# Performance work log

Hardware: AMD Instinct MI355X
Metric: run time of the kernel (lower is better)

## Reference

```python
import jax, jax.numpy as jnp
import numpy as np

N, E, F_IN, C, H, G = 50000, 800000, 128, 64, 4, 512

def _gat_layer(x, src, dst, W, a_src, a_dst, b):
    # x: [N, Fin]; W: [Fin, H*C]; a_src/a_dst: [H, C]; b: [C]
    n = x.shape[0]
    h = (x @ W).reshape(n, H, C)                      # [N,H,C]
    al_s = jnp.einsum('nhc,hc->nh', h, a_src)         # [N,H]
    al_d = jnp.einsum('nhc,hc->nh', h, a_dst)
    alpha = jax.nn.leaky_relu(al_s[src] + al_d[dst], 0.2)   # [Et,H]
    m = jax.ops.segment_max(alpha, dst, num_segments=n)      # segment softmax over dst
    e = jnp.exp(alpha - m[dst])
    s = jax.ops.segment_sum(e, dst, num_segments=n)
    coef = e / (s[dst] + 1e-16)                        # [Et,H]
    msg = h[src] * coef[:, :, None]                    # [Et,H,C]
    out = jax.ops.segment_sum(msg, dst, num_segments=n)
    return out.mean(axis=1) + b                        # concat=False: average heads

def setup_inputs():
    key = jax.random.key(0)
    ks = jax.random.split(key, 24)
    x = jax.random.normal(ks[0], (N, F_IN), jnp.float32)
    edge_index = jax.random.randint(ks[1], (2, E), 0, N, jnp.int64)
    edge_attr = jax.random.normal(ks[2], (E, 4), jnp.float32)
    batch_index = jnp.sort(jax.random.randint(ks[3], (N,), 0, G, jnp.int64))
    p = lambda k, shp: jax.random.normal(k, shp, jnp.float32) * 0.05
    inp = {
        'x': x, 'edge_index': edge_index, 'edge_attr': edge_attr, 'batch_index': batch_index,
        'W0': p(ks[4], (F_IN, H * C)), 'as0': p(ks[5], (H, C)), 'ad0': p(ks[6], (H, C)), 'b0': jnp.zeros((C,), jnp.float32),
        'W1': p(ks[7], (C, H * C)), 'as1': p(ks[8], (H, C)), 'ad1': p(ks[9], (H, C)), 'b1': jnp.zeros((C,), jnp.float32),
        'W2': p(ks[10], (C, H * C)), 'as2': p(ks[11], (H, C)), 'ad2': p(ks[12], (H, C)), 'b2': jnp.zeros((C,), jnp.float32),
        'Wr1': p(ks[13], (2 * C, C)), 'br1': jnp.zeros((C,), jnp.float32),
        'Wr2': p(ks[14], (C, 1)), 'br2': jnp.zeros((1,), jnp.float32),
    }
    return inp

def reference(x, edge_index, edge_attr, batch_index,
              W0, as0, ad0, b0, W1, as1, ad1, b1, W2, as2, ad2, b2,
              Wr1, br1, Wr2, br2):
    # add self-loops (PyG GATConv default add_self_loops=True); edge_attr unused (edge_dim=None)
    loop = jnp.arange(N, dtype=edge_index.dtype)
    src = jnp.concatenate([edge_index[0], loop])
    dst = jnp.concatenate([edge_index[1], loop])
    h = jax.nn.leaky_relu(_gat_layer(x, src, dst, W0, as0, ad0, b0))
    h = jax.nn.leaky_relu(_gat_layer(h, src, dst, W1, as1, ad1, b1))
    h = jax.nn.leaky_relu(_gat_layer(h, src, dst, W2, as2, ad2, b2))
    gmp = jax.ops.segment_max(h, batch_index, num_segments=G)           # [G,C]
    cnt = jax.ops.segment_sum(jnp.ones((N,), h.dtype), batch_index, num_segments=G)
    gap = jax.ops.segment_sum(h, batch_index, num_segments=G) / jnp.maximum(cnt, 1.0)[:, None]
    hid = jnp.concatenate([gmp, gap], axis=1)                            # [G,2C]
    hid = jax.nn.leaky_relu(hid @ Wr1 + br1)
    return hid @ Wr2 + br2                                               # [G,1]
```

## Files before the change

kernel.cpp:

```cpp
#include <hip/hip_runtime.h>
#include <hip/hip_bf16.h>
#include <hip/hip_fp16.h>

#define NN   50000
#define EE   800000
#define FIN  128
#define CC   64
#define HH   4
#define GG   512
#define CAP  64

__device__ __forceinline__ float leaky02(float x) { return x >= 0.f ? x : 0.2f * x; }
__device__ __forceinline__ float leaky01(float x) { return x >= 0.f ? x : 0.01f * x; }

__global__ __launch_bounds__(256) void build_csr(const int* __restrict__ ei,
                                                 int* __restrict__ deg,
                                                 int* __restrict__ csr) {
    int e = blockIdx.x * 256 + threadIdx.x;
    if (e >= EE) return;
    int s = ei[e];
    int d = ei[EE + e];
    if ((unsigned)d >= NN || (unsigned)s >= NN) return;
    int pos = atomicAdd(&deg[d], 1);
    if (pos < CAP) csr[d * CAP + pos] = s;
}

template <int K>
__global__ __launch_bounds__(256, 3) void gemm_gat(const float* __restrict__ x,
                                                   const float* __restrict__ W,
                                                   const float* __restrict__ a_src,
                                                   const float* __restrict__ a_dst,
                                                   __half* __restrict__ h_out,
                                                   float* __restrict__ al_s,
                                                   float* __restrict__ al_d) {
    __shared__ float Xs[32 * 128];
    __shared__ float Ws[32 * 128];
    const int t  = threadIdx.x;
    const int tc = t & 15;
    const int tr = t >> 4;
    const int r0 = blockIdx.x * 128;
    const int c0 = blockIdx.y * 128;

    float acc[8][8];
#pragma unroll
    for (int i = 0; i < 8; ++i)
#pragma unroll
        for (int j = 0; j < 8; ++j) acc[i][j] = 0.f;

    for (int k0 = 0; k0 < K; k0 += 32) {
#pragma unroll
        for (int jj = 0; jj < 4; ++jj) {
            int id = t + jj * 256;
            int m  = id >> 3;
            int k4 = id & 7;
            int row = r0 + m;
            row = row < NN ? row : NN - 1;
            float4 v = *(const float4*)(x + (size_t)row * K + k0 + k4 * 4);
#pragma unroll
            for (int c = 0; c < 4; ++c) {
                int k = k4 * 4 + c;
                int slot = (m >> 3) ^ (k >> 2);
                Xs[k * 128 + slot * 8 + (m & 7)] = ((const float*)&v)[c];
            }
        }
#pragma unroll
        for (int jj = 0; jj < 4; ++jj) {
            int id = t + jj * 256;
            int k  = id >> 5;
            int n4 = id & 31;
            float4 v = *(const float4*)(W + (size_t)(k0 + k) * 256 + c0 + n4 * 4);
            *(float4*)(Ws + k * 128 + n4 * 4) = v;
        }
        __syncthreads();

#pragma unroll
        for (int k = 0; k < 32; ++k) {
            int aslot = tr ^ (k >> 2);
            const float* ax = &Xs[k * 128 + aslot * 8];
            const float* bw = &Ws[k * 128 + tc * 8];
            float a0[8], b0[8];
            *(float4*)&a0[0] = *(const float4*)&ax[0];
            *(float4*)&a0[4] = *(const float4*)&ax[4];
            *(float4*)&b0[0] = *(const float4*)&bw[0];
            *(float4*)&b0[4] = *(const float4*)&bw[4];
#pragma unroll
            for (int i = 0; i < 8; ++i)
#pragma unroll
                for (int j = 0; j < 8; ++j)
                    acc[i][j] = fmaf(a0[i], b0[j], acc[i][j]);
        }
        __syncthreads();
    }

    const int colbase = c0 + tc * 8;
    const int head = colbase >> 6;
    float as_c[8], ad_c[8];
#pragma unroll
    for (int j = 0; j < 8; ++j) {
        as_c[j] = a_src[colbase + j];
        ad_c[j] = a_dst[colbase + j];
    }
#pragma unroll
    for (int i = 0; i < 8; ++i) {
        int row = r0 + tr * 8 + i;
        bool ok = row < NN;
        if (ok) {
            __half2 p0 = __floats2half2_rn(acc[i][0], acc[i][1]);
            __half2 p1 = __floats2half2_rn(acc[i][2], acc[i][3]);
            __half2 p2 = __floats2half2_rn(acc[i][4], acc[i][5]);
            __half2 p3 = __floats2half2_rn(acc[i][6], acc[i][7]);
            uint4 pk;
            pk.x = *(unsigned int*)&p0;
            pk.y = *(unsigned int*)&p1;
            pk.z = *(unsigned int*)&p2;
            pk.w = *(unsigned int*)&p3;
            *(uint4*)(h_out + (size_t)row * 256 + colbase) = pk;
        }
        float ps = 0.f, pd = 0.f;
#pragma unroll
        for (int j = 0; j < 8; ++j) {
            ps = fmaf(acc[i][j], as_c[j], ps);
            pd = fmaf(acc[i][j], ad_c[j], pd);
        }
#pragma unroll
        for (int off = 1; off <= 4; off <<= 1) {
            ps += __shfl_xor(ps, off, 64);
            pd += __shfl_xor(pd, off, 64);
        }
        if (ok && (tc & 7) == 0) {
            al_s[(size_t)row * 4 + head] = ps;
            al_d[(size_t)row * 4 + head] = pd;
        }
    }
}

struct Half4 { __half2 a, b; };

__global__ __launch_bounds__(256) void gat_aggregate(const __half* __restrict__ h_buf,
                                                     const float* __restrict__ al_s,
                                                     const float* __restrict__ al_d,
                                                     const int* __restrict__ deg,
                                                     const int* __restrict__ csr,
                                                     const float* __restrict__ bias,
                                                     float* __restrict__ xout) {
    __shared__ __align__(16) float els[4][64][4];
    const int w    = threadIdx.x >> 6;
    const int lane = threadIdx.x & 63;
    const int n    = blockIdx.x * 4 + w;
    if (n >= NN) return;
    const int d = min(deg[n], CAP);

    float4 ad4 = *(const float4*)(al_d + (size_t)n * 4);
    float4 as4 = *(const float4*)(al_s + (size_t)n * 4);
    const float* adp = (const float*)&ad4;
    const float* asp = (const float*)&as4;

    float aself[4];
#pragma unroll
    for (int h = 0; h < 4; ++h) aself[h] = leaky02(asp[h] + adp[h]);

    int s_lane = 0;
    float a_lane[4];
    if (lane < d) {
        s_lane = csr[(size_t)n * CAP + lane];
        float4 s4 = *(const float4*)(al_s + (size_t)s_lane * 4);
        const float* sp = (const float*)&s4;
#pragma unroll
        for (int h = 0; h < 4; ++h) a_lane[h] = leaky02(sp[h] + adp[h]);
    } else {
#pragma unroll
        for (int h = 0; h < 4; ++h) a_lane[h] = -INFINITY;
    }

    float mx[4];
#pragma unroll
    for (int h = 0; h < 4; ++h) {
        mx[h] = fmaxf(aself[h], a_lane[h]);
#pragma unroll
        for (int off = 32; off; off >>= 1) mx[h] = fmaxf(mx[h], __shfl_xor(mx[h], off, 64));
    }

    float e[4], sm[4];
#pragma unroll
    for (int h = 0; h < 4; ++h) {
        e[h] = (lane < d) ? expf(a_lane[h] - mx[h]) : 0.f;
        sm[h] = e[h];
#pragma unroll
        for (int off = 32; off; off >>= 1) sm[h] += __shfl_xor(sm[h], off, 64);
    }
    float eself[4], inv[4];
    float4 coef;
    float* cf = (float*)&coef;
#pragma unroll
    for (int h = 0; h < 4; ++h) {
        eself[h] = expf(aself[h] - mx[h]);
        inv[h] = 1.f / (sm[h] + eself[h] + 1e-16f);
        cf[h] = e[h] * inv[h];
    }
    *(float4*)&els[w][lane][0] = coef;

    const int hh = lane >> 4;
    const __half* __restrict__ hb = h_buf + (size_t)lane * 4;
    const float selfc = eself[hh] * inv[hh];
    Half4 hv = *(const Half4*)(hb + (size_t)n * 256);
    float2 f0 = __half22float2(hv.a);
    float2 f1 = __half22float2(hv.b);
    float acc0 = f0.x * selfc, acc1 = f0.y * selfc, acc2 = f1.x * selfc, acc3 = f1.y * selfc;

    for (int j = 0; j < d; ++j) {
        int s = __shfl(s_lane, j, 64);
        float cj = els[w][j][hh];
        Half4 hj = *(const Half4*)(hb + (size_t)s * 256);
        float2 g0 = __half22float2(hj.a);
        float2 g1 = __half22float2(hj.b);
        acc0 = fmaf(g0.x, cj, acc0);
        acc1 = fmaf(g0.y, cj, acc1);
        acc2 = fmaf(g1.x, cj, acc2);
        acc3 = fmaf(g1.y, cj, acc3);
    }

#pragma unroll
    for (int off = 16; off <= 32; off <<= 1) {
        acc0 += __shfl_xor(acc0, off, 64);
        acc1 += __shfl_xor(acc1, off, 64);
        acc2 += __shfl_xor(acc2, off, 64);
        acc3 += __shfl_xor(acc3, off, 64);
    }
    if (lane < 16) {
        float4 o;
        o.x = leaky01(acc0 * 0.25f + bias[lane * 4 + 0]);
        o.y = leaky01(acc1 * 0.25f + bias[lane * 4 + 1]);
        o.z = leaky01(acc2 * 0.25f + bias[lane * 4 + 2]);
        o.w = leaky01(acc3 * 0.25f + bias[lane * 4 + 3]);
        *(float4*)(xout + (size_t)n * 64 + lane * 4) = o;
    }
}

__global__ __launch_bounds__(256) void readout(const float* __restrict__ x,
                                               const int* __restrict__ batch,
                                               float* __restrict__ gmp,
                                               float* __restrict__ gap) {
    int g = blockIdx.x;
    int a = 0, b = NN;
    while (a < b) { int m = (a + b) >> 1; if (batch[m] < g) a = m + 1; else b = m; }
    int lo = a;
    a = lo; b = NN;
    while (a < b) { int m = (a + b) >> 1; if (batch[m] < g + 1) a = m + 1; else b = m; }
    int hi = a;

    int t = threadIdx.x, c = t & 63, s = t >> 6;
    float mx = -INFINITY, sm = 0.f;
    for (int n = lo + s; n < hi; n += 4) {
        float v = x[(size_t)n * 64 + c];
        mx = fmaxf(mx, v);
        sm += v;
    }
    __shared__ float smx[256], ssm[256];
    smx[t] = mx; ssm[t] = sm;
    __syncthreads();
    if (t < 64) {
        mx = fmaxf(fmaxf(smx[t], smx[t + 64]), fmaxf(smx[t + 128], smx[t + 192]));
        sm = ssm[t] + ssm[t + 64] + ssm[t + 128] + ssm[t + 192];
        int cnt = hi - lo;
        gmp[g * 64 + t] = mx;
        gap[g * 64 + t] = sm / fmaxf((float)cnt, 1.0f);
    }
}

__global__ __launch_bounds__(64) void mlp_readout(const float* __restrict__ gmp,
                                                  const float* __restrict__ gap,
                                                  const float* __restrict__ Wr1,
                                                  const float* __restrict__ br1,
                                                  const float* __restrict__ Wr2,
                                                  const float* __restrict__ br2,
                                                  float* __restrict__ out) {
    int g = blockIdx.x;
    int j = threadIdx.x;
    double acc = (double)br1[j];
    for (int i = 0; i < 64; ++i) acc += (double)gmp[g * 64 + i] * (double)Wr1[i * 64 + j];
    for (int i = 0; i < 64; ++i) acc += (double)gap[g * 64 + i] * (double)Wr1[(64 + i) * 64 + j];
    float v = (float)acc;
    v = v >= 0.f ? v : 0.01f * v;
    double tv = (double)v * (double)Wr2[j];
#pragma unroll
    for (int off = 32; off; off >>= 1) tv += __shfl_xor(tv, off, 64);
    if (j == 0) out[g] = (float)(tv + (double)br2[0]);
}

extern "C" void kernel_launch(void* const* d_in, const int* in_sizes, int n_in,
                              void* d_out, int out_size, void* d_ws, size_t ws_size,
                              hipStream_t stream) {
    const float* x   = (const float*)d_in[0];
    const int* ei    = (const int*)d_in[1];
    const int* batch = (const int*)d_in[3];
    const float* W0  = (const float*)d_in[4];
    const float* as0 = (const float*)d_in[5];
    const float* ad0 = (const float*)d_in[6];
    const float* b0  = (const float*)d_in[7];
    const float* W1  = (const float*)d_in[8];
    const float* as1 = (const float*)d_in[9];
    const float* ad1 = (const float*)d_in[10];
    const float* b1  = (const float*)d_in[11];
    const float* W2  = (const float*)d_in[12];
    const float* as2 = (const float*)d_in[13];
    const float* ad2 = (const float*)d_in[14];
    const float* b2  = (const float*)d_in[15];
    const float* Wr1 = (const float*)d_in[16];
    const float* br1 = (const float*)d_in[17];
    const float* Wr2 = (const float*)d_in[18];
    const float* br2 = (const float*)d_in[19];
    float* out = (float*)d_out;

    __half* h_buf = (__half*)d_ws;
    float* al_s  = (float*)(h_buf + (size_t)NN * 256);
    float* al_d  = al_s + (size_t)NN * 4;
    float* xbuf  = al_d + (size_t)NN * 4;
    float* gmp   = xbuf + (size_t)NN * 64;
    float* gap   = gmp + (size_t)GG * 64;
    int*   deg   = (int*)(gap + (size_t)GG * 64);
    int*   csr   = deg + NN;

    hipMemsetAsync(deg, 0, NN * sizeof(int), stream);
    build_csr<<<(EE + 255) / 256, 256, 0, stream>>>(ei, deg, csr);

    const dim3 gemm_grid((NN + 127) / 128, 2);
    const int agg_grid = (NN + 3) / 4;

    gemm_gat<FIN><<<gemm_grid, 256, 0, stream>>>(x, W0, as0, ad0, h_buf, al_s, al_d);
    gat_aggregate<<<agg_grid, 256, 0, stream>>>(h_buf, al_s, al_d, deg, csr, b0, xbuf);
    gemm_gat<CC><<<gemm_grid, 256, 0, stream>>>(xbuf, W1, as1, ad1, h_buf, al_s, al_d);
    gat_aggregate<<<agg_grid, 256, 0, stream>>>(h_buf, al_s, al_d, deg, csr, b1, xbuf);
    gemm_gat<CC><<<gemm_grid, 256, 0, stream>>>(xbuf, W2, as2, ad2, h_buf, al_s, al_d);
    gat_aggregate<<<agg_grid, 256, 0, stream>>>(h_buf, al_s, al_d, deg, csr, b2, xbuf);

    readout<<<GG, 256, 0, stream>>>(xbuf, batch, gmp, gap);
    mlp_readout<<<GG, 64, 0, stream>>>(gmp, gap, Wr1, br1, Wr2, br2, out);
}
```

Before: 529.9 us.

## Aggregate neighbors in half2 with two edges per wave iteration

Rewrites the GAT aggregation loop so each half-wave handles a different edge and each lane loads 8 halves (16 bytes) per neighbor, halving the number of loop iterations. Softmax coefficients are stored as half2 in shared memory and accumulated with packed half FMA, with the self-loop folded in as edge 0. This cuts loop overhead and instruction count per gathered row but accumulates in fp16, which risks precision loss. The n>=NN early return is removed, which is safe only because NN is divisible by 4.

```diff
diff --git a/kernel.cpp b/kernel.cpp
--- a/kernel.cpp
+++ b/kernel.cpp
@@ -134,7 +134,7 @@
     }
 }
 
-struct Half4 { __half2 a, b; };
+struct Half8 { __half2 h[4]; };
 
 __global__ __launch_bounds__(256) void gat_aggregate(const __half* __restrict__ h_buf,
                                                      const float* __restrict__ al_s,
@@ -143,11 +143,10 @@
                                                      const int* __restrict__ csr,
                                                      const float* __restrict__ bias,
                                                      float* __restrict__ xout) {
-    __shared__ __align__(16) float els[4][64][4];
+    __shared__ __align__(16) __half2 els[4][66][4];
     const int w    = threadIdx.x >> 6;
     const int lane = threadIdx.x & 63;
     const int n    = blockIdx.x * 4 + w;
-    if (n >= NN) return;
     const int d = min(deg[n], CAP);
 
     float4 ad4 = *(const float4*)(al_d + (size_t)n * 4);
@@ -189,50 +188,81 @@
         for (int off = 32; off; off >>= 1) sm[h] += __shfl_xor(sm[h], off, 64);
     }
     float eself[4], inv[4];
-    float4 coef;
-    float* cf = (float*)&coef;
 #pragma unroll
     for (int h = 0; h < 4; ++h) {
         eself[h] = expf(aself[h] - mx[h]);
         inv[h] = 1.f / (sm[h] + eself[h] + 1e-16f);
-        cf[h] = e[h] * inv[h];
-    }
-    *(float4*)&els[w][lane][0] = coef;
-
-    const int hh = lane >> 4;
-    const __half* __restrict__ hb = h_buf + (size_t)lane * 4;
-    const float selfc = eself[hh] * inv[hh];
-    Half4 hv = *(const Half4*)(hb + (size_t)n * 256);
-    float2 f0 = __half22float2(hv.a);
-    float2 f1 = __half22float2(hv.b);
-    float acc0 = f0.x * selfc, acc1 = f0.y * selfc, acc2 = f1.x * selfc, acc3 = f1.y * selfc;
-
-    for (int j = 0; j < d; ++j) {
-        int s = __shfl(s_lane, j, 64);
-        float cj = els[w][j][hh];
-        Half4 hj = *(const Half4*)(hb + (size_t)s * 256);
-        float2 g0 = __half22float2(hj.a);
-        float2 g1 = __half22float2(hj.b);
-        acc0 = fmaf(g0.x, cj, acc0);
-        acc1 = fmaf(g0.y, cj, acc1);
-        acc2 = fmaf(g1.x, cj, acc2);
-        acc3 = fmaf(g1.y, cj, acc3);
-    }
-
-#pragma unroll
-    for (int off = 16; off <= 32; off <<= 1) {
-        acc0 += __shfl_xor(acc0, off, 64);
-        acc1 += __shfl_xor(acc1, off, 64);
-        acc2 += __shfl_xor(acc2, off, 64);
-        acc3 += __shfl_xor(acc3, off, 64);
-    }
-    if (lane < 16) {
-        float4 o;
-        o.x = leaky01(acc0 * 0.25f + bias[lane * 4 + 0]);
-        o.y = leaky01(acc1 * 0.25f + bias[lane * 4 + 1]);
-        o.z = leaky01(acc2 * 0.25f + bias[lane * 4 + 2]);
-        o.w = leaky01(acc3 * 0.25f + bias[lane * 4 + 3]);
-        *(float4*)(xout + (size_t)n * 64 + lane * 4) = o;
+    }
+    if (lane < d) {
+#pragma unroll
+        for (int h = 0; h < 4; ++h) {
+            float c = e[h] * inv[h];
+            els[w][lane + 1][h] = __floats2half2_rn(c, c);
+        }
+    }
+    if (lane == 0) {
+#pragma unroll
+        for (int h = 0; h < 4; ++h) {
+            float c = eself[h] * inv[h];
+            els[w][0][h] = __floats2half2_rn(c, c);
+        }
+    }
+
+    const int q    = lane >> 5;
+    const int m    = lane & 31;
+    const int head = m >> 3;
+    const __half* __restrict__ hb = h_buf + m * 8;
+
+    __half2 z = __floats2half2_rn(0.f, 0.f);
+    __half2 acc0 = z, acc1 = z, acc2 = z, acc3 = z;
+    const int count = d + 1;
+    for (int t2 = 0; 2 * t2 < count; ++t2) {
+        int v = 2 * t2 + q;
+        int vi = v > 0 ? v - 1 : 0;
+        int s = __shfl(s_lane, vi, 64);
+        s = v == 0 ? n : s;
+        if (v < count) {
+            __half2 c2 = els[w][v][head];
+            Half8 r = *(const Half8*)(hb + (size_t)s * 256);
+            acc0 = __hfma2(r.h[0], c2, acc0);
+            acc1 = __hfma2(r.h[1], c2, acc1);
+            acc2 = __hfma2(r.h[2], c2, acc2);
+            acc3 = __hfma2(r.h[3], c2, acc3);
+        }
+    }
+
+    int i0 = __shfl_xor(*(int*)&acc0, 32, 64);
+    int i1 = __shfl_xor(*(int*)&acc1, 32, 64);
+    int i2 = __shfl_xor(*(int*)&acc2, 32, 64);
+    int i3 = __shfl_xor(*(int*)&acc3, 32, 64);
+    acc0 = __hadd2(acc0, *(__half2*)&i0);
+    acc1 = __hadd2(acc1, *(__half2*)&i1);
+    acc2 = __hadd2(acc2, *(__half2*)&i2);
+    acc3 = __hadd2(acc3, *(__half2*)&i3);
+
+    float ch[8];
+    float2 f;
+    f = __half22float2(acc0); ch[0] = f.x; ch[1] = f.y;
+    f = __half22float2(acc1); ch[2] = f.x; ch[3] = f.y;
+    f = __half22float2(acc2); ch[4] = f.x; ch[5] = f.y;
+    f = __half22float2(acc3); ch[6] = f.x; ch[7] = f.y;
+#pragma unroll
+    for (int k = 0; k < 8; ++k) {
+        ch[k] += __shfl_xor(ch[k], 8, 64);
+        ch[k] += __shfl_xor(ch[k], 16, 64);
+    }
+    if (lane < 8) {
+        float4 o0, o1;
+        o0.x = leaky01(ch[0] * 0.25f + bias[lane * 8 + 0]);
+        o0.y = leaky01(ch[1] * 0.25f + bias[lane * 8 + 1]);
+        o0.z = leaky01(ch[2] * 0.25f + bias[lane * 8 + 2]);
+        o0.w = leaky01(ch[3] * 0.25f + bias[lane * 8 + 3]);
+        o1.x = leaky01(ch[4] * 0.25f + bias[lane * 8 + 4]);
+        o1.y = leaky01(ch[5] * 0.25f + bias[lane * 8 + 5]);
+        o1.z = leaky01(ch[6] * 0.25f + bias[lane * 8 + 6]);
+        o1.w = leaky01(ch[7] * 0.25f + bias[lane * 8 + 7]);
+        *(float4*)(xout + (size_t)n * 64 + lane * 8)     = o0;
+        *(float4*)(xout + (size_t)n * 64 + lane * 8 + 4) = o1;
     }
 }
 
```

Result: faster. 502.7 us (-5.1%).
